# Kernel optimization log

Hardware: AMD Instinct MI355X
Metric: run time of the kernel (lower is better)

Reference implementation:

```python
import jax, jax.numpy as jnp
import numpy as np

B = 384          # batch; must equal F for the final broadcast to be valid
F = 384          # out_features
H = 64           # hidden_dim
TAU = 1.0        # d_k passed to attention()
EPS = 1e-12      # F.normalize eps


def _l2_normalize(x):
    # torch F.normalize(p=2, dim=-1): x / max(||x||, eps)
    n = jnp.sqrt(jnp.sum(x * x, axis=-1, keepdims=True))
    return x / jnp.maximum(n, EPS)


def setup_inputs() -> dict:
    key = jax.random.key(0)
    kx, kwq, kbq, kwk, kbk = jax.random.split(key, 5)
    bound = 1.0 / np.sqrt(F)  # torch Linear default init range
    x = jax.random.normal(kx, (B, F), dtype=jnp.float32)
    Wq = jax.random.uniform(kwq, (F * H, F), jnp.float32, -bound, bound)
    bq = jax.random.uniform(kbq, (F * H,), jnp.float32, -bound, bound)
    Wk = jax.random.uniform(kwk, (F * H, F), jnp.float32, -bound, bound)
    bk = jax.random.uniform(kbk, (F * H,), jnp.float32, -bound, bound)
    return {"x": x, "Wq": Wq, "bq": bq, "Wk": Wk, "bk": bk}


def reference(x, Wq, bq, Wk, bk):
    # q = qs(x), k = ks(x): [B, F*H] -> reshape [B, F, H]
    q = (x @ Wq.T + bq).reshape(B, F, H)
    k = (x @ Wk.T + bk).reshape(B, F, H)
    # L2-normalized QK attention with temperature sqrt(tau)
    q = _l2_normalize(q)
    k = _l2_normalize(k)
    scores = jnp.einsum('bfh,bgh->bfg', q, k) / jnp.sqrt(jnp.float32(TAU))
    scores = jax.nn.softmax(scores, axis=-1)  # [B, F, F]
    # faithful to `input * scores`: x[B,F] left-pads to [1,B,F]; valid since B==F
    return x * scores
```

## Files before the change

### kernel.cpp

```cpp
#include <hip/hip_runtime.h>
#include <hip/hip_bf16.h>


typedef __attribute__((ext_vector_type(8))) short bf16x8;
typedef __attribute__((ext_vector_type(4))) float f32x4;

__device__ __forceinline__ ushort f2bf(float f) {
  union { __hip_bfloat16 h; ushort u; } c;
  c.h = __float2bfloat16(f);
  return c.u;
}

__device__ __forceinline__ void load_lds16(const void* g, void* l) {
  __builtin_amdgcn_global_load_lds(
      (const __attribute__((address_space(1))) void*)g,
      (__attribute__((address_space(3))) void*)l, 16, 0, 0);
}

__global__ __launch_bounds__(256) void xconv(const float* __restrict__ xin,
                                             ushort* __restrict__ xbf) {
  int t = blockIdx.x * 256 + threadIdx.x;
  int o = t * 8;
  int kt = o / 12288;
  int rem = o - kt * 12288;
  int m = rem >> 5;
  int sp = (rem >> 3) & 3;
  int slot = sp ^ ((m >> 1) & 3);
  const float* src = xin + m * 384 + kt * 32 + slot * 8;
  float4 a = *reinterpret_cast<const float4*>(src);
  float4 b = *reinterpret_cast<const float4*>(src + 4);
  ushort4 u0 = make_ushort4(f2bf(a.x), f2bf(a.y), f2bf(a.z), f2bf(a.w));
  ushort4 u1 = make_ushort4(f2bf(b.x), f2bf(b.y), f2bf(b.z), f2bf(b.w));
  *reinterpret_cast<ushort4*>(xbf + o)     = u0;
  *reinterpret_cast<ushort4*>(xbf + o + 4) = u1;
}

__global__ __launch_bounds__(256) void qk_gemm(
    const ushort* __restrict__ xbf,
    const float* __restrict__ Wq, const float* __restrict__ bq,
    const float* __restrict__ Wk, const float* __restrict__ bk,
    ushort* __restrict__ qhat, ushort* __restrict__ khat)
{
  const int bx = blockIdx.x;
  const int n0 = bx * 64;
  const float* W    = blockIdx.y ? Wk : Wq;
  const float* bias = blockIdx.y ? bk : bq;
  ushort* outp      = blockIdx.y ? khat : qhat;

  __shared__ __align__(16) ushort Alds[384 * 32];
  __shared__ __align__(16) ushort Blds[64 * 40];

  const int tid  = threadIdx.x;
  const int wave = tid >> 6;
  const int lane = tid & 63;
  const int l15  = lane & 15;
  const int lhi  = lane >> 4;

  f32x4 acc[6][4];
  #pragma unroll
  for (int m = 0; m < 6; ++m)
    #pragma unroll
    for (int n = 0; n < 4; ++n) acc[m][n] = (f32x4)(0.f);

  const int aslot = lhi ^ ((l15 >> 1) & 3);

  for (int kt = 0; kt < 12; ++kt) {
    const ushort* asrc = xbf + kt * 12288 + lane * 8;
    #pragma unroll
    for (int i = 0; i < 6; ++i) {
      int chunk = wave * 6 + i;
      load_lds16(asrc + chunk * 512, (char*)Alds + chunk * 1024);
    }
    #pragma unroll
    for (int i = 0; i < 2; ++i) {
      int idx = tid + 256 * i;
      int row = idx >> 3, c4 = idx & 7;
      float4 v = *reinterpret_cast<const float4*>(
          W + (size_t)(n0 + row) * 384 + kt * 32 + c4 * 4);
      ushort4 u = make_ushort4(f2bf(v.x), f2bf(v.y), f2bf(v.z), f2bf(v.w));
      *reinterpret_cast<ushort4*>(&Blds[row * 40 + c4 * 4]) = u;
    }
    __syncthreads();

    bf16x8 bfr[4];
    #pragma unroll
    for (int nf = 0; nf < 4; ++nf)
      bfr[nf] = *reinterpret_cast<const bf16x8*>(&Blds[(nf * 16 + l15) * 40 + lhi * 8]);
    #pragma unroll
    for (int mf = 0; mf < 6; ++mf) {
      int rr = wave * 96 + mf * 16 + l15;
      bf16x8 afr = *reinterpret_cast<const bf16x8*>(&Alds[rr * 32 + aslot * 8]);
      #pragma unroll
      for (int nf = 0; nf < 4; ++nf)
        acc[mf][nf] = __builtin_amdgcn_mfma_f32_16x16x32_bf16(afr, bfr[nf], acc[mf][nf], 0, 0, 0);
    }
    __syncthreads();
  }

  float bv[4];
  int hp[4];
  const int sw = bx & 7;
  #pragma unroll
  for (int nf = 0; nf < 4; ++nf) {
    bv[nf] = bias[n0 + nf * 16 + l15];
    hp[nf] = (((nf * 2 + (l15 >> 3)) ^ sw) << 3) + (l15 & 7);
  }

  #pragma unroll
  for (int mf = 0; mf < 6; ++mf) {
    float ss[4];
    #pragma unroll
    for (int j = 0; j < 4; ++j) {
      float s = 0.f;
      #pragma unroll
      for (int nf = 0; nf < 4; ++nf) {
        float v = acc[mf][nf][j] + bv[nf];
        acc[mf][nf][j] = v;
        s += v * v;
      }
      ss[j] = s;
    }
    #pragma unroll
    for (int m = 1; m < 16; m <<= 1) {
      #pragma unroll
      for (int j = 0; j < 4; ++j) ss[j] += __shfl_xor(ss[j], m, 64);
    }
    #pragma unroll
    for (int j = 0; j < 4; ++j) {
      float scale = 1.f / fmaxf(sqrtf(ss[j]), 1e-12f);
      int row = wave * 96 + mf * 16 + lhi * 4 + j;
      #pragma unroll
      for (int nf = 0; nf < 4; ++nf)
        outp[(size_t)row * 24576 + n0 + hp[nf]] = f2bf(acc[mf][nf][j] * scale);
    }
  }
}

#define PSTR 396
__global__ __launch_bounds__(256) void attn_out(
    const float* __restrict__ xin,
    const ushort* __restrict__ qhat,
    const ushort* __restrict__ khat,
    float* __restrict__ out)
{
  const int f0 = blockIdx.x * 32;
  const int b  = blockIdx.y;

  __shared__ __align__(16) char smem[32 * PSTR * 4];
  ushort* Klds = reinterpret_cast<ushort*>(smem);
  float*  Slds = reinterpret_cast<float*>(smem);
  __shared__ float redmax[128], redsum[128], mfin[32], invs[32];

  const int tid  = threadIdx.x;
  const int wave = tid >> 6;
  const int lane = tid & 63;
  const int l15  = lane & 15;
  const int lhi  = lane >> 4;

  const ushort* ksrc = khat + (size_t)b * 24576 + lane * 8;
  #pragma unroll
  for (int i = 0; i < 12; ++i) {
    int chunk = wave * 12 + i;
    load_lds16(ksrc + chunk * 512, smem + chunk * 1024);
  }

  bf16x8 aq[2][2];
  #pragma unroll
  for (int mf = 0; mf < 2; ++mf)
    #pragma unroll
    for (int ks = 0; ks < 2; ++ks)
      aq[mf][ks] = *reinterpret_cast<const bf16x8*>(
          qhat + (size_t)b * 24576 + (f0 + mf * 16 + l15) * 64 +
          (((ks * 4 + lhi) ^ (l15 & 7)) << 3));
  __syncthreads();

  f32x4 acc[2][6];
  #pragma unroll
  for (int m = 0; m < 2; ++m)
    #pragma unroll
    for (int n = 0; n < 6; ++n) acc[m][n] = (f32x4)(0.f);

  #pragma unroll
  for (int ks = 0; ks < 2; ++ks) {
    #pragma unroll
    for (int nf = 0; nf < 6; ++nf) {
      int rr = wave * 96 + nf * 16 + l15;
      bf16x8 bk8 = *reinterpret_cast<const bf16x8*>(
          &Klds[rr * 64 + (((ks * 4 + lhi) ^ (l15 & 7)) << 3)]);
      #pragma unroll
      for (int mf = 0; mf < 2; ++mf)
        acc[mf][nf] = __builtin_amdgcn_mfma_f32_16x16x32_bf16(aq[mf][ks], bk8, acc[mf][nf], 0, 0, 0);
    }
  }

  #pragma unroll
  for (int mf = 0; mf < 2; ++mf) {
    #pragma unroll
    for (int j = 0; j < 4; ++j) {
      float m = acc[mf][0][j];
      #pragma unroll
      for (int nf = 1; nf < 6; ++nf) m = fmaxf(m, acc[mf][nf][j]);
      #pragma unroll
      for (int s = 1; s < 16; s <<= 1) m = fmaxf(m, __shfl_xor(m, s, 64));
      if (l15 == 0) redmax[wave * 32 + mf * 16 + lhi * 4 + j] = m;
    }
  }
  __syncthreads();
  if (tid < 32)
    mfin[tid] = fmaxf(fmaxf(redmax[tid], redmax[32 + tid]),
                      fmaxf(redmax[64 + tid], redmax[96 + tid]));
  __syncthreads();

  #pragma unroll
  for (int mf = 0; mf < 2; ++mf) {
    #pragma unroll
    for (int j = 0; j < 4; ++j) {
      int r = mf * 16 + lhi * 4 + j;
      float m = mfin[r];
      float s = 0.f;
      #pragma unroll
      for (int nf = 0; nf < 6; ++nf) {
        float p = __expf(acc[mf][nf][j] - m);
        Slds[r * PSTR + wave * 96 + nf * 16 + l15] = p;
        s += p;
      }
      #pragma unroll
      for (int sh = 1; sh < 16; sh <<= 1) s += __shfl_xor(s, sh, 64);
      if (l15 == 0) redsum[wave * 32 + r] = s;
    }
  }
  __syncthreads();
  if (tid < 32)
    invs[tid] = 1.f / (redsum[tid] + redsum[32 + tid] + redsum[64 + tid] + redsum[96 + tid]);
  __syncthreads();

  #pragma unroll
  for (int i = 0; i < 12; ++i) {
    int idx = tid + 256 * i;
    int row = idx / 96, c = idx - row * 96;
    float iv = invs[row];
    float4 p4 = *reinterpret_cast<const float4*>(&Slds[row * PSTR + c * 4]);
    float4 x4 = *reinterpret_cast<const float4*>(xin + (size_t)(f0 + row) * 384 + c * 4);
    float4 o;
    o.x = x4.x * p4.x * iv;  o.y = x4.y * p4.y * iv;
    o.z = x4.z * p4.z * iv;  o.w = x4.w * p4.w * iv;
    *reinterpret_cast<float4*>(out + (size_t)b * 147456 + (size_t)(f0 + row) * 384 + c * 4) = o;
  }
}

extern "C" void kernel_launch(void* const* d_in, const int* in_sizes, int n_in,
                              void* d_out, int out_size, void* d_ws, size_t ws_size,
                              hipStream_t stream) {
  const float* x  = (const float*)d_in[0];
  const float* Wq = (const float*)d_in[1];
  const float* bq = (const float*)d_in[2];
  const float* Wk = (const float*)d_in[3];
  const float* bk = (const float*)d_in[4];
  float* out = (float*)d_out;

  ushort* qhat = (ushort*)d_ws;
  ushort* khat = qhat + (size_t)384 * 24576;
  ushort* xbf  = khat + (size_t)384 * 24576;

  xconv<<<dim3(72), dim3(256), 0, stream>>>(x, xbf);

  dim3 g1(384, 2), b1(256);
  qk_gemm<<<g1, b1, 0, stream>>>(xbf, Wq, bq, Wk, bk, qhat, khat);

  dim3 g2(12, 384), b2(256);
  attn_out<<<g2, b2, 0, stream>>>(x, qhat, khat, out);
}
```

Measured before the change: 126.5 us.

## Restructure attention kernel so each wave owns full score rows in registers

After: 175.3 us. 1.39x slower.

```diff
diff --git a/kernel.cpp b/kernel.cpp
--- a/kernel.cpp
+++ b/kernel.cpp
@@ -136,20 +136,19 @@
   }
 }
 
-#define PSTR 396
-__global__ __launch_bounds__(256) void attn_out(
+__global__ __launch_bounds__(256, 3) void attn_out(
     const float* __restrict__ xin,
     const ushort* __restrict__ qhat,
     const ushort* __restrict__ khat,
     float* __restrict__ out)
 {
-  const int f0 = blockIdx.x * 32;
-  const int b  = blockIdx.y;
-
-  __shared__ __align__(16) char smem[32 * PSTR * 4];
-  ushort* Klds = reinterpret_cast<ushort*>(smem);
-  float*  Slds = reinterpret_cast<float*>(smem);
-  __shared__ float redmax[128], redsum[128], mfin[32], invs[32];
+  const int id = blockIdx.x;
+  const int xcd = id & 7;
+  const int j_  = id >> 3;
+  const int b   = xcd * 48 + j_ / 6;
+  const int f0  = (j_ % 6) * 64;
+
+  __shared__ __align__(16) ushort Klds[384 * 64];
 
   const int tid  = threadIdx.x;
   const int wave = tid >> 6;
@@ -161,90 +160,69 @@
   #pragma unroll
   for (int i = 0; i < 12; ++i) {
     int chunk = wave * 12 + i;
-    load_lds16(ksrc + chunk * 512, smem + chunk * 1024);
-  }
-
-  bf16x8 aq[2][2];
-  #pragma unroll
-  for (int mf = 0; mf < 2; ++mf)
-    #pragma unroll
-    for (int ks = 0; ks < 2; ++ks)
-      aq[mf][ks] = *reinterpret_cast<const bf16x8*>(
-          qhat + (size_t)b * 24576 + (f0 + mf * 16 + l15) * 64 +
-          (((ks * 4 + lhi) ^ (l15 & 7)) << 3));
+    load_lds16(ksrc + chunk * 512, (char*)Klds + chunk * 1024);
+  }
+
+  const int fr = f0 + wave * 16 + l15;
+  bf16x8 q8[2];
+  #pragma unroll
+  for (int ks = 0; ks < 2; ++ks)
+    q8[ks] = *reinterpret_cast<const bf16x8*>(
+        qhat + (size_t)b * 24576 + (size_t)fr * 64 + (((ks * 4 + lhi) ^ (l15 & 7)) << 3));
   __syncthreads();
 
-  f32x4 acc[2][6];
-  #pragma unroll
-  for (int m = 0; m < 2; ++m)
-    #pragma unroll
-    for (int n = 0; n < 6; ++n) acc[m][n] = (f32x4)(0.f);
+  f32x4 acc[24];
+  #pragma unroll
+  for (int n = 0; n < 24; ++n) acc[n] = (f32x4)(0.f);
 
   #pragma unroll
   for (int ks = 0; ks < 2; ++ks) {
     #pragma unroll
-    for (int nf = 0; nf < 6; ++nf) {
-      int rr = wave * 96 + nf * 16 + l15;
-      bf16x8 bk8 = *reinterpret_cast<const bf16x8*>(
-          &Klds[rr * 64 + (((ks * 4 + lhi) ^ (l15 & 7)) << 3)]);
-      #pragma unroll
-      for (int mf = 0; mf < 2; ++mf)
-        acc[mf][nf] = __builtin_amdgcn_mfma_f32_16x16x32_bf16(aq[mf][ks], bk8, acc[mf][nf], 0, 0, 0);
-    }
-  }
-
-  #pragma unroll
-  for (int mf = 0; mf < 2; ++mf) {
-    #pragma unroll
-    for (int j = 0; j < 4; ++j) {
-      float m = acc[mf][0][j];
-      #pragma unroll
-      for (int nf = 1; nf < 6; ++nf) m = fmaxf(m, acc[mf][nf][j]);
-      #pragma unroll
-      for (int s = 1; s < 16; s <<= 1) m = fmaxf(m, __shfl_xor(m, s, 64));
-      if (l15 == 0) redmax[wave * 32 + mf * 16 + lhi * 4 + j] = m;
-    }
-  }
-  __syncthreads();
-  if (tid < 32)
-    mfin[tid] = fmaxf(fmaxf(redmax[tid], redmax[32 + tid]),
-                      fmaxf(redmax[64 + tid], redmax[96 + tid]));
-  __syncthreads();
-
-  #pragma unroll
-  for (int mf = 0; mf < 2; ++mf) {
-    #pragma unroll
-    for (int j = 0; j < 4; ++j) {
-      int r = mf * 16 + lhi * 4 + j;
-      float m = mfin[r];
-      float s = 0.f;
-      #pragma unroll
-      for (int nf = 0; nf < 6; ++nf) {
-        float p = __expf(acc[mf][nf][j] - m);
-        Slds[r * PSTR + wave * 96 + nf * 16 + l15] = p;
-        s += p;
-      }
-      #pragma unroll
-      for (int sh = 1; sh < 16; sh <<= 1) s += __shfl_xor(s, sh, 64);
-      if (l15 == 0) redsum[wave * 32 + r] = s;
-    }
-  }
-  __syncthreads();
-  if (tid < 32)
-    invs[tid] = 1.f / (redsum[tid] + redsum[32 + tid] + redsum[64 + tid] + redsum[96 + tid]);
-  __syncthreads();
-
-  #pragma unroll
-  for (int i = 0; i < 12; ++i) {
-    int idx = tid + 256 * i;
-    int row = idx / 96, c = idx - row * 96;
-    float iv = invs[row];
-    float4 p4 = *reinterpret_cast<const float4*>(&Slds[row * PSTR + c * 4]);
-    float4 x4 = *reinterpret_cast<const float4*>(xin + (size_t)(f0 + row) * 384 + c * 4);
+    for (int nf = 0; nf < 24; ++nf) {
+      bf16x8 kf = *reinterpret_cast<const bf16x8*>(
+          &Klds[(nf * 16 + l15) * 64 + (((ks * 4 + lhi) ^ (l15 & 7)) << 3)]);
+      acc[nf] = __builtin_amdgcn_mfma_f32_16x16x32_bf16(kf, q8[ks], acc[nf], 0, 0, 0);
+    }
+  }
+
+  float m0 = acc[0][0], m1 = acc[0][1], m2 = acc[0][2], m3 = acc[0][3];
+  #pragma unroll
+  for (int nf = 1; nf < 24; ++nf) {
+    m0 = fmaxf(m0, acc[nf][0]); m1 = fmaxf(m1, acc[nf][1]);
+    m2 = fmaxf(m2, acc[nf][2]); m3 = fmaxf(m3, acc[nf][3]);
+  }
+  float m = fmaxf(fmaxf(m0, m1), fmaxf(m2, m3));
+  m = fmaxf(m, __shfl_xor(m, 16, 64));
+  m = fmaxf(m, __shfl_xor(m, 32, 64));
+
+  float s0 = 0.f, s1 = 0.f, s2 = 0.f, s3 = 0.f;
+  #pragma unroll
+  for (int nf = 0; nf < 24; ++nf) {
+    float p0 = __expf(acc[nf][0] - m);
+    float p1 = __expf(acc[nf][1] - m);
+    float p2 = __expf(acc[nf][2] - m);
+    float p3 = __expf(acc[nf][3] - m);
+    acc[nf][0] = p0; acc[nf][1] = p1; acc[nf][2] = p2; acc[nf][3] = p3;
+    s0 += p0; s1 += p1; s2 += p2; s3 += p3;
+  }
+  float s = (s0 + s1) + (s2 + s3);
+  s += __shfl_xor(s, 16, 64);
+  s += __shfl_xor(s, 32, 64);
+  const float inv = 1.f / s;
+
+  const float* xrow = xin + (size_t)fr * 384;
+  float* orow = out + (size_t)b * 147456 + (size_t)fr * 384;
+  const int c0 = lhi * 4;
+  #pragma unroll 4
+  for (int nf = 0; nf < 24; ++nf) {
+    int c = nf * 16 + c0;
+    float4 x4 = *reinterpret_cast<const float4*>(xrow + c);
     float4 o;
-    o.x = x4.x * p4.x * iv;  o.y = x4.y * p4.y * iv;
-    o.z = x4.z * p4.z * iv;  o.w = x4.w * p4.w * iv;
-    *reinterpret_cast<float4*>(out + (size_t)b * 147456 + (size_t)(f0 + row) * 384 + c * 4) = o;
+    o.x = x4.x * acc[nf][0] * inv;
+    o.y = x4.y * acc[nf][1] * inv;
+    o.z = x4.z * acc[nf][2] * inv;
+    o.w = x4.w * acc[nf][3] * inv;
+    *reinterpret_cast<float4*>(orow + c) = o;
   }
 }
 
@@ -267,6 +245,5 @@
   dim3 g1(384, 2), b1(256);
   qk_gemm<<<g1, b1, 0, stream>>>(xbf, Wq, bq, Wk, bk, qhat, khat);
 
-  dim3 g2(12, 384), b2(256);
-  attn_out<<<g2, b2, 0, stream>>>(x, qhat, khat, out);
-}
+  attn_out<<<dim3(2304), dim3(256), 0, stream>>>(x, qhat, khat, out);
+}
```
